# Kernel tuning notes

Measured on AMD Instinct MI355X. Metric: run time of the kernel, lower is better.

The kernel has to match this reference:

```python
import jax, jax.numpy as jnp
import numpy as np

N = 10000        # nodes
E = 160000       # edges (before self loops)
F_IN = 4         # n_features
D = 128          # d_model (per-head out channels for GAT, GCN width)
H = 8            # n_heads
NEG_SLOPE = 0.2  # PyG GATConv default leaky relu slope


def setup_inputs() -> dict:
    key = jax.random.key(0)
    ks = jax.random.split(key, 10)
    x = jax.random.normal(ks[0], (N, F_IN), dtype=jnp.float32)
    edge_index = jax.random.randint(ks[1], (2, E), 0, N, dtype=jnp.int64)
    s = 0.05
    gat_w = jax.random.normal(ks[2], (F_IN, H * D), dtype=jnp.float32) * s
    att_src = jax.random.normal(ks[3], (H, D), dtype=jnp.float32) * s
    att_dst = jax.random.normal(ks[4], (H, D), dtype=jnp.float32) * s
    gat_b = jnp.zeros((H * D,), dtype=jnp.float32)
    gcn1_w = jax.random.normal(ks[5], (H * D, D), dtype=jnp.float32) * s
    gcn1_b = jnp.zeros((D,), dtype=jnp.float32)
    gcn2_w = jax.random.normal(ks[6], (D, D), dtype=jnp.float32) * s
    gcn2_b = jnp.zeros((D,), dtype=jnp.float32)
    return {"x": x, "edge_index": edge_index, "gat_w": gat_w,
            "att_src": att_src, "att_dst": att_dst, "gat_b": gat_b,
            "gcn1_w": gcn1_w, "gcn1_b": gcn1_b,
            "gcn2_w": gcn2_w, "gcn2_b": gcn2_b}


def _add_self_loops(edge_index, n):
    loops = jnp.arange(n, dtype=edge_index.dtype)
    src = jnp.concatenate([edge_index[0], loops])
    dst = jnp.concatenate([edge_index[1], loops])
    return src, dst


def _gat_conv(x, src, dst, w, att_src, att_dst, b):
    # PyG GATConv, concat=True: h [N,H,D]
    h = (x @ w).reshape(-1, H, D)
    a_s = jnp.einsum('nhd,hd->nh', h, att_src)   # per-node src score
    a_d = jnp.einsum('nhd,hd->nh', h, att_dst)   # per-node dst score
    e = jax.nn.leaky_relu(a_s[src] + a_d[dst], NEG_SLOPE)  # [Etot,H]
    # segment softmax over destination node, per head
    m = jax.ops.segment_max(e, dst, num_segments=N)
    ex = jnp.exp(e - m[dst])
    denom = jax.ops.segment_sum(ex, dst, num_segments=N)
    alpha = ex / denom[dst]                       # [Etot,H]
    msg = h[src] * alpha[:, :, None]              # [Etot,H,D]
    out = jax.ops.segment_sum(msg, dst, num_segments=N)  # [N,H,D]
    return out.reshape(-1, H * D) + b


def _gcn_conv(x, src, dst, w, b):
    # PyG GCNConv with symmetric normalization (self loops already added)
    h = x @ w
    deg = jax.ops.segment_sum(jnp.ones_like(dst, dtype=h.dtype), dst,
                              num_segments=N)
    dinv = jnp.where(deg > 0, jax.lax.rsqrt(deg), 0.0)
    norm = dinv[src] * dinv[dst]                  # [Etot]
    out = jax.ops.segment_sum(h[src] * norm[:, None], dst, num_segments=N)
    return out + b


def reference(x, edge_index, gat_w, att_src, att_dst, gat_b,
              gcn1_w, gcn1_b, gcn2_w, gcn2_b):
    src, dst = _add_self_loops(edge_index, N)
    h = _gat_conv(x, src, dst, gat_w, att_src, att_dst, gat_b)
    h = jax.nn.gelu(h, approximate=False)         # torch F.gelu is exact erf
    h = _gcn_conv(h, src, dst, gcn1_w, gcn1_b)
    h = jax.nn.gelu(h, approximate=False)
    h = _gcn_conv(h, src, dst, gcn2_w, gcn2_b)
    return h                                      # [N, D]
```

## Files before the change

### kernel.cpp

```cpp
#include <hip/hip_runtime.h>
#include <math.h>

#define HEADS 8
#define DHEAD 128
#define CMODEL 1024
#define BCAP 64

typedef __attribute__((ext_vector_type(8))) short bf16x8;
typedef __attribute__((ext_vector_type(4))) float f32x4;

__device__ __forceinline__ float gelu_exact(float x) {
    return 0.5f * x * (1.0f + erff(x * 0.70710678118654752440f));
}

__device__ __forceinline__ unsigned short f2bf(float f) {
    unsigned u = __float_as_uint(f);
    return (unsigned short)((u + 0x7FFFu + ((u >> 16) & 1u)) >> 16);
}
__device__ __forceinline__ float bf2f(unsigned short h) {
    return __uint_as_float((unsigned)h << 16);
}

__global__ void __launch_bounds__(256) k_scores(const float* __restrict__ x,
                                                const float* __restrict__ gat_w,
                                                const float* __restrict__ att_src,
                                                const float* __restrict__ att_dst,
                                                const float* __restrict__ W1,
                                                const float* __restrict__ W2,
                                                float* __restrict__ xpack,
                                                float* __restrict__ a_d,
                                                int* __restrict__ cursor,
                                                unsigned short* __restrict__ W1hi,
                                                unsigned short* __restrict__ W1lo,
                                                unsigned short* __restrict__ W2hi,
                                                unsigned short* __restrict__ W2lo,
                                                int n_nodes, int nb_scores) {
    if ((int)blockIdx.x >= nb_scores) {
        int t = (blockIdx.x - nb_scores) * 256 + threadIdx.x;
        const int total1 = (1024 >> 5) * 8 * 64;
        const int total2 = (128 >> 5) * 8 * 64;
        const float* W; unsigned short *Whi, *Wlo;
        if (t < total1) { W = W1; Whi = W1hi; Wlo = W1lo; }
        else if (t < total1 + total2) { t -= total1; W = W2; Whi = W2hi; Wlo = W2lo; }
        else return;
        int lane = t & 63;
        int ct = (t >> 6) & 7;
        int kc = t >> 9;
        int quad = lane >> 4;
        int col = ct * 16 + (lane & 15);
        size_t o = (size_t)t * 8;
        #pragma unroll
        for (int j = 0; j < 8; j++) {
            float w = W[(size_t)(kc * 32 + quad * 8 + j) * 128 + col];
            unsigned short h = f2bf(w);
            Whi[o + j] = h;
            Wlo[o + j] = f2bf(w - bf2f(h));
        }
        return;
    }
    __shared__ float ws_s[32], ws_d[32];
    int t = threadIdx.x;
    if (t < 64) {
        int e = t >> 1;
        int which = t & 1;
        int hh = e >> 2, k = e & 3;
        const float* wrow = gat_w + k * CMODEL + hh * DHEAD;
        const float* av = which ? (att_dst + hh * DHEAD) : (att_src + hh * DHEAD);
        float s = 0.0f;
        for (int c = 0; c < DHEAD; c++) s += wrow[c] * av[c];
        if (which) ws_d[e] = s; else ws_s[e] = s;
    }
    int gid = blockIdx.x * 256 + t;
    if (gid < n_nodes) cursor[gid] = 0;
    __syncthreads();
    int p = gid;
    if (p >= n_nodes * HEADS) return;
    int n = p >> 3, hh = p & 7;
    float4 xv = *(const float4*)(x + (size_t)n * 4);
    float4 ws = *(const float4*)&ws_s[hh * 4];
    float4 wd = *(const float4*)&ws_d[hh * 4];
    a_d[p] = xv.x * wd.x + xv.y * wd.y + xv.z * wd.z + xv.w * wd.w;
    xpack[(size_t)n * 16 + 4 + hh] =
        xv.x * ws.x + xv.y * ws.y + xv.z * ws.z + xv.w * ws.w;
    if (hh == 0) *(float4*)(xpack + (size_t)n * 16) = xv;
}

__global__ void __launch_bounds__(256) k_scatter(const int* __restrict__ ei,
                                                 int* __restrict__ cursor,
                                                 int* __restrict__ bucket,
                                                 int n_nodes, int n_edges) {
    int e = blockIdx.x * 256 + threadIdx.x;
    int etot = n_edges + n_nodes;
    if (e >= etot) return;
    int s, d;
    if (e < n_edges) { s = ei[e]; d = ei[n_edges + e]; }
    else             { s = d = e - n_edges; }
    int pos = atomicAdd(&cursor[d], 1);
    if (pos < BCAP) bucket[(d << 6) + pos] = s;
}

__global__ void __launch_bounds__(256, 3) k_smax_mm1(const float* __restrict__ xpack,
                                                  const float* __restrict__ a_d,
                                                  const int* __restrict__ deg,
                                                  const int* __restrict__ bucket,
                                                  const float* __restrict__ gat_w,
                                                  const float* __restrict__ gat_b,
                                                  const unsigned short* __restrict__ Bhi,
                                                  const unsigned short* __restrict__ Blo,
                                                  float* __restrict__ t,
                                                  int n_nodes) {
    __shared__ float xs[16 * 32];
    __shared__ float ck[2][16 * 68];
    int mb = blockIdx.x;
    int tid = threadIdx.x;
    int lane = tid & 63;
    int w = tid >> 6;

    bf16x8 bhA[2][2], blA[2][2], bhB[2][2], blB[2][2];
    #pragma unroll
    for (int kc2 = 0; kc2 < 2; kc2++)
        #pragma unroll
        for (int ct = 0; ct < 2; ct++) {
            size_t bi = (((size_t)(kc2 * 8) + w * 2 + ct) * 64 + lane) * 8;
            bhA[kc2][ct] = *(const bf16x8*)(Bhi + bi);
            blA[kc2][ct] = *(const bf16x8*)(Blo + bi);
        }

    {
        int q = tid >> 1;
        int half = tid & 1;
        int ln = tid >> 4, hh = q & 7;
        int n = mb * 16 + ln;
        int nc = (n < n_nodes) ? n : (n_nodes - 1);
        int grp = lane & 48;
        int gl = lane & 15;
        int basec = nc << 6;
        int pre0 = bucket[basec + gl];
        int pre1 = bucket[basec + 16 + gl];
        int pre2 = bucket[basec + 32 + gl];
        int pre3 = bucket[basec + 48 + gl];
        auto SRC = [&](int e) -> int {
            int v = (e < 16) ? pre0 : (e < 32) ? pre1 : (e < 48) ? pre2 : pre3;
            return __shfl(v, grp + (e & 15), 64);
        };
        float sum = 0.0f;
        float4 acc = make_float4(0, 0, 0, 0);
        if (n < n_nodes) {
            int dg = deg[n]; if (dg > BCAP) dg = BCAP;
            float ad = a_d[n * 8 + hh];
            int r = half;
            for (; r + 6 < dg; r += 8) {
                int s0 = SRC(r + 0), s1 = SRC(r + 2);
                int s2 = SRC(r + 4), s3 = SRC(r + 6);
                const float* p0 = xpack + (size_t)s0 * 16;
                const float* p1 = xpack + (size_t)s1 * 16;
                const float* p2 = xpack + (size_t)s2 * 16;
                const float* p3 = xpack + (size_t)s3 * 16;
                float e0 = p0[4 + hh] + ad, e1 = p1[4 + hh] + ad;
                float e2 = p2[4 + hh] + ad, e3 = p3[4 + hh] + ad;
                float4 x0 = *(const float4*)p0;
                float4 x1 = *(const float4*)p1;
                float4 x2 = *(const float4*)p2;
                float4 x3 = *(const float4*)p3;
                e0 = (e0 > 0.0f) ? e0 : 0.2f * e0;  float w0 = __expf(e0);
                e1 = (e1 > 0.0f) ? e1 : 0.2f * e1;  float w1 = __expf(e1);
                e2 = (e2 > 0.0f) ? e2 : 0.2f * e2;  float w2 = __expf(e2);
                e3 = (e3 > 0.0f) ? e3 : 0.2f * e3;  float w3 = __expf(e3);
                sum += w0 + w1 + w2 + w3;
                acc.x += w0 * x0.x + w1 * x1.x + w2 * x2.x + w3 * x3.x;
                acc.y += w0 * x0.y + w1 * x1.y + w2 * x2.y + w3 * x3.y;
                acc.z += w0 * x0.z + w1 * x1.z + w2 * x2.z + w3 * x3.z;
                acc.w += w0 * x0.w + w1 * x1.w + w2 * x2.w + w3 * x3.w;
            }
            for (; r < dg; r += 2) {
                int s = SRC(r);
                const float* ps = xpack + (size_t)s * 16;
                float e = ps[4 + hh] + ad;
                e = (e > 0.0f) ? e : 0.2f * e;
                float ex = __expf(e);
                float4 xv = *(const float4*)ps;
                sum += ex;
                acc.x += ex * xv.x; acc.y += ex * xv.y;
                acc.z += ex * xv.z; acc.w += ex * xv.w;
            }
        }
        sum   += __shfl_down(sum, 1);
        acc.x += __shfl_down(acc.x, 1);
        acc.y += __shfl_down(acc.y, 1);
        acc.z += __shfl_down(acc.z, 1);
        acc.w += __shfl_down(acc.w, 1);
        if (half == 0) {
            float inv = (sum > 0.0f) ? (1.0f / sum) : 0.0f;
            *(float4*)&xs[q * 4] = make_float4(acc.x * inv, acc.y * inv,
                                               acc.z * inv, acc.w * inv);
        }
    }
    __syncthreads();

    int lm = lane & 15, quad = lane >> 4;
    int cc = tid & 63;
    int rp = tid >> 6;
    f32x4 macc[2];
    macc[0] = (f32x4){0.0f, 0.0f, 0.0f, 0.0f};
    macc[1] = (f32x4){0.0f, 0.0f, 0.0f, 0.0f};

#define ROUND(RR, BH, BL, BH_N, BL_N, RNEXT)                                    \
    {                                                                           \
        int buf = (RR) & 1;                                                     \
        int col = (RR) * 64 + cc;                                               \
        float w0 = gat_w[col], w1 = gat_w[1024 + col],                          \
              w2 = gat_w[2048 + col], w3 = gat_w[3072 + col];                   \
        float bb = gat_b[col];                                                  \
        int hh2 = (RR) >> 1;                                                    \
        _Pragma("unroll")                                                       \
        for (int rr = 0; rr < 4; rr++) {                                        \
            int row = rp * 4 + rr;                                              \
            float4 xa = *(const float4*)&xs[(row * 8 + hh2) * 4];               \
            float v = xa.x * w0 + xa.y * w1 + xa.z * w2 + xa.w * w3 + bb;       \
            ck[buf][row * 68 + cc] = gelu_exact(v);                             \
        }                                                                       \
        _Pragma("unroll")                                                       \
        for (int kc2 = 0; kc2 < 2; kc2++)                                       \
            _Pragma("unroll")                                                   \
            for (int ct = 0; ct < 2; ct++) {                                    \
                size_t bi = (((size_t)((RNEXT) * 2 + kc2) * 8 + w * 2 + ct) * 64 + lane) * 8; \
                BH_N[kc2][ct] = *(const bf16x8*)(Bhi + bi);                     \
                BL_N[kc2][ct] = *(const bf16x8*)(Blo + bi);                     \
            }                                                                   \
        asm volatile("s_waitcnt lgkmcnt(0)" ::: "memory");                      \
        __builtin_amdgcn_s_barrier();                                           \
        __builtin_amdgcn_sched_barrier(0);                                      \
        _Pragma("unroll")                                                       \
        for (int kc2 = 0; kc2 < 2; kc2++) {                                     \
            float a[8];                                                         \
            *(float4*)&a[0] = *(const float4*)&ck[buf][lm * 68 + kc2 * 32 + quad * 8];     \
            *(float4*)&a[4] = *(const float4*)&ck[buf][lm * 68 + kc2 * 32 + quad * 8 + 4]; \
            bf16x8 ah, al;                                                      \
            _Pragma("unroll")                                                   \
            for (int j = 0; j < 8; j++) {                                       \
                unsigned short h = f2bf(a[j]);                                  \
                ah[j] = (short)h;                                               \
                al[j] = (short)f2bf(a[j] - bf2f(h));                            \
            }                                                                   \
            _Pragma("unroll")                                                   \
            for (int ct = 0; ct < 2; ct++) {                                    \
                macc[ct] = __builtin_amdgcn_mfma_f32_16x16x32_bf16(ah, BH[kc2][ct], macc[ct], 0, 0, 0); \
                macc[ct] = __builtin_amdgcn_mfma_f32_16x16x32_bf16(al, BH[kc2][ct], macc[ct], 0, 0, 0); \
                macc[ct] = __builtin_amdgcn_mfma_f32_16x16x32_bf16(ah, BL[kc2][ct], macc[ct], 0, 0, 0); \
            }                                                                   \
        }                                                                       \
    }

    for (int r = 0; r < 16; r += 2) {
        ROUND(r,     bhA, blA, bhB, blB, r + 1);
        ROUND(r + 1, bhB, blB, bhA, blA, (r + 2 < 16 ? r + 2 : 15));
    }
#undef ROUND

    #pragma unroll
    for (int ct = 0; ct < 2; ct++) {
        int col = (w * 2 + ct) * 16 + lm;
        #pragma unroll
        for (int reg = 0; reg < 4; reg++) {
            int row = mb * 16 + quad * 4 + reg;
            if (row < n_nodes) {
                float dv = 1.0f / sqrtf((float)deg[row]);
                t[(size_t)row * 128 + col] = macc[ct][reg] * dv;
            }
        }
    }
}

__global__ void __launch_bounds__(256) k_mm_mfma(const unsigned short* __restrict__ Afrag_hi,
                                                 const unsigned short* __restrict__ Afrag_lo,
                                                 const unsigned short* __restrict__ Bhi,
                                                 const unsigned short* __restrict__ Blo,
                                                 const int* __restrict__ deg_scale,
                                                 float* __restrict__ outp,
                                                 int n_nodes, int n_mtiles, int kcn) {
    int lane = threadIdx.x & 63;
    int w = threadIdx.x >> 6;
    int colhalf = w >> 1;
    int mtile = blockIdx.x * 2 + (w & 1);
    if (mtile >= n_mtiles) return;

    int lm = lane & 15, quad = lane >> 4;
    f32x4 acc[4];
    #pragma unroll
    for (int ct = 0; ct < 4; ct++) acc[ct] = (f32x4){0.0f, 0.0f, 0.0f, 0.0f};

    const unsigned short* ah_p = Afrag_hi + ((size_t)mtile * kcn * 64 + lane) * 8;
    const unsigned short* al_p = Afrag_lo + ((size_t)mtile * kcn * 64 + lane) * 8;
    const unsigned short* bh_p = Bhi + ((size_t)(colhalf * 4) * 64 + lane) * 8;
    const unsigned short* bl_p = Blo + ((size_t)(colhalf * 4) * 64 + lane) * 8;

    #pragma unroll 4
    for (int kci = 0; kci < kcn; kci++) {
        bf16x8 ah = *(const bf16x8*)(ah_p + (size_t)kci * 512);
        bf16x8 al = *(const bf16x8*)(al_p + (size_t)kci * 512);
        #pragma unroll
        for (int ct = 0; ct < 4; ct++) {
            bf16x8 bh = *(const bf16x8*)(bh_p + (size_t)kci * 4096 + ct * 512);
            bf16x8 bl = *(const bf16x8*)(bl_p + (size_t)kci * 4096 + ct * 512);
            acc[ct] = __builtin_amdgcn_mfma_f32_16x16x32_bf16(ah, bh, acc[ct], 0, 0, 0);
            acc[ct] = __builtin_amdgcn_mfma_f32_16x16x32_bf16(al, bh, acc[ct], 0, 0, 0);
            acc[ct] = __builtin_amdgcn_mfma_f32_16x16x32_bf16(ah, bl, acc[ct], 0, 0, 0);
        }
    }
    #pragma unroll
    for (int ct = 0; ct < 4; ct++) {
        int col = (colhalf * 4 + ct) * 16 + lm;
        #pragma unroll
        for (int reg = 0; reg < 4; reg++) {
            int row = mtile * 16 + quad * 4 + reg;
            if (row < n_nodes) {
                float v = acc[ct][reg] * (1.0f / sqrtf((float)deg_scale[row]));
                outp[(size_t)row * 128 + col] = v;
            }
        }
    }
}

__global__ void __launch_bounds__(256) k_gcn_agg(const float* __restrict__ t,
                                                 const int* __restrict__ deg,
                                                 const int* __restrict__ bucket,
                                                 const float* __restrict__ bias,
                                                 float* __restrict__ outF,
                                                 unsigned short* __restrict__ outHi,
                                                 unsigned short* __restrict__ outLo,
                                                 int n_nodes, int mode) {
    int c = threadIdx.x & 31;
    int ln = threadIdx.x >> 5;
    int n = blockIdx.x * 8 + ln;
    int col0 = blockIdx.y * 64;
    if (n >= n_nodes) return;
    float2 acc = make_float2(0.0f, 0.0f);
    int dgt = deg[n];
    int dg = dgt > BCAP ? BCAP : dgt;
    int base = n << 6;
    int sa = bucket[base + c];
    int sb = bucket[base + 32 + c];
    const float* tp = t + col0 + c * 2;
    int d1 = dg > 32 ? 32 : dg;
    int r = 0;
    for (; r + 4 <= d1; r += 4) {
        int s0 = __shfl(sa, r + 0, 32);
        int s1 = __shfl(sa, r + 1, 32);
        int s2 = __shfl(sa, r + 2, 32);
        int s3 = __shfl(sa, r + 3, 32);
        float2 v0 = *(const float2*)(tp + (size_t)s0 * 128);
        float2 v1 = *(const float2*)(tp + (size_t)s1 * 128);
        float2 v2 = *(const float2*)(tp + (size_t)s2 * 128);
        float2 v3 = *(const float2*)(tp + (size_t)s3 * 128);
        acc.x += v0.x + v1.x + v2.x + v3.x;
        acc.y += v0.y + v1.y + v2.y + v3.y;
    }
    for (; r < d1; r++) {
        int s = __shfl(sa, r, 32);
        float2 v = *(const float2*)(tp + (size_t)s * 128);
        acc.x += v.x; acc.y += v.y;
    }
    for (; r < dg; r++) {
        int s = __shfl(sb, r - 32, 32);
        float2 v = *(const float2*)(tp + (size_t)s * 128);
        acc.x += v.x; acc.y += v.y;
    }
    float dn = 1.0f / sqrtf((float)dgt);
    int k = col0 + c * 2;
    float2 bb = *(const float2*)(bias + k);
    float vx = acc.x * dn + bb.x;
    float vy = acc.y * dn + bb.y;
    if (mode) {
        vx = gelu_exact(vx); vy = gelu_exact(vy);
        size_t o = (((size_t)(n >> 4) * 4 + (k >> 5)) * 64
                    + ((k >> 3) & 3) * 16 + (n & 15)) * 8 + (k & 7);
        unsigned short hx = f2bf(vx), hy = f2bf(vy);
        outHi[o] = hx; outHi[o + 1] = hy;
        outLo[o] = f2bf(vx - bf2f(hx));
        outLo[o + 1] = f2bf(vy - bf2f(hy));
    } else {
        *(float2*)(outF + (size_t)n * 128 + k) = make_float2(vx, vy);
    }
}

extern "C" void kernel_launch(void* const* d_in, const int* in_sizes, int n_in,
                              void* d_out, int out_size, void* d_ws, size_t ws_size,
                              hipStream_t stream) {
    const float* x        = (const float*)d_in[0];
    const int*   ei       = (const int*)d_in[1];
    const float* gat_w    = (const float*)d_in[2];
    const float* att_src  = (const float*)d_in[3];
    const float* att_dst  = (const float*)d_in[4];
    const float* gat_b    = (const float*)d_in[5];
    const float* gcn1_w   = (const float*)d_in[6];
    const float* gcn1_b   = (const float*)d_in[7];
    const float* gcn2_w   = (const float*)d_in[8];
    const float* gcn2_b   = (const float*)d_in[9];
    float* out = (float*)d_out;

    int N = in_sizes[0] / 4;
    int E = in_sizes[1] / 2;
    int Etot = E + N;
    int n_mtiles = (N + 15) / 16;

    char* base = (char*)d_ws;
    float*          t      = (float*)(base);
    float*          t2     = (float*)(base + 5120000);
    unsigned short* out2hi = (unsigned short*)(base + 10240000);
    unsigned short* out2lo = (unsigned short*)(base + 12800000);
    unsigned short* w1hi   = (unsigned short*)(base + 26000000);
    unsigned short* w1lo   = (unsigned short*)(base + 26262144);
    unsigned short* w2hi   = (unsigned short*)(base + 26524288);
    unsigned short* w2lo   = (unsigned short*)(base + 26557056);
    size_t off = 81920000;
    float* xpack  = (float*)(base + off); off += (size_t)N * 16 * 4;
    float* a_d    = (float*)(base + off); off += (size_t)N * 8 * 4;
    int*   cursor = (int*)(base + off);   off += (size_t)N * 4;
    int*   bucket = (int*)(base + off);   off += (size_t)N * BCAP * 4;

    int nb_scores = (N * HEADS + 255) / 256;
    int nb_wswz   = (16384 + 2048 + 255) / 256;

    k_scores<<<nb_scores + nb_wswz, 256, 0, stream>>>(x, gat_w, att_src, att_dst,
                                                      gcn1_w, gcn2_w, xpack, a_d, cursor,
                                                      w1hi, w1lo, w2hi, w2lo, N, nb_scores);

    k_scatter<<<(Etot + 255) / 256, 256, 0, stream>>>(ei, cursor, bucket, N, E);

    k_smax_mm1<<<n_mtiles, 256, 0, stream>>>(xpack, a_d, cursor, bucket,
                                             gat_w, gat_b, w1hi, w1lo, t, N);

    int nmb2 = (n_mtiles + 1) / 2;
    int nagg = (N + 7) / 8;

    k_gcn_agg<<<dim3(nagg, 2), 256, 0, stream>>>(t, cursor, bucket, gcn1_b,
                                                 nullptr, out2hi, out2lo, N, 1);

    k_mm_mfma<<<dim3(nmb2, 1), 256, 0, stream>>>(out2hi, out2lo, w2hi, w2lo,
                                                 cursor, t2, N, n_mtiles, 4);

    k_gcn_agg<<<dim3(nagg, 2), 256, 0, stream>>>(t2, cursor, bucket, gcn2_b,
                                                 out, nullptr, nullptr, N, 0);
}
```

Measured before the change: 157.0 us.

## Split GAT softmax aggregation out of the first GEMM kernel

Moves the GAT edge-softmax aggregation from the fused k_smax_mm1 into a separate k_gat_agg kernel. The new kernel uses 4 threads per (node, head) instead of 2, and writes the aggregated 4-feature inputs to a workspace buffer. k_mm1 then just loads that tile into shared memory. The goal is more parallelism for the gather part and less register pressure in the MFMA kernel. The cost is an extra launch and a small global round trip.

```diff
diff --git a/kernel.cpp b/kernel.cpp
--- a/kernel.cpp
+++ b/kernel.cpp
@@ -99,16 +99,94 @@
     if (pos < BCAP) bucket[(d << 6) + pos] = s;
 }
 
-__global__ void __launch_bounds__(256, 3) k_smax_mm1(const float* __restrict__ xpack,
-                                                  const float* __restrict__ a_d,
-                                                  const int* __restrict__ deg,
-                                                  const int* __restrict__ bucket,
-                                                  const float* __restrict__ gat_w,
-                                                  const float* __restrict__ gat_b,
-                                                  const unsigned short* __restrict__ Bhi,
-                                                  const unsigned short* __restrict__ Blo,
-                                                  float* __restrict__ t,
-                                                  int n_nodes) {
+__global__ void __launch_bounds__(256) k_gat_agg(const float* __restrict__ xpack,
+                                                 const float* __restrict__ a_d,
+                                                 const int* __restrict__ deg,
+                                                 const int* __restrict__ bucket,
+                                                 float* __restrict__ xagg,
+                                                 int n_nodes) {
+    int tid = threadIdx.x;
+    int lane = tid & 63;
+    int ln = tid >> 5;
+    int g = lane & 31;
+    int hh = g >> 2;
+    int quarter = g & 3;
+    int n = blockIdx.x * 8 + ln;
+    int nc = (n < n_nodes) ? n : (n_nodes - 1);
+    int basec = nc << 6;
+    int sa = bucket[basec + g];
+    int sb = bucket[basec + 32 + g];
+    int grp = lane & 32;
+    auto SRC = [&](int e) -> int {
+        int v = (e < 32) ? sa : sb;
+        return __shfl(v, grp + (e & 31), 64);
+    };
+    float sum = 0.0f;
+    float4 acc = make_float4(0, 0, 0, 0);
+    if (n < n_nodes) {
+        int dg = deg[n]; if (dg > BCAP) dg = BCAP;
+        float ad = a_d[n * 8 + hh];
+        int r = quarter;
+        for (; r + 12 < dg; r += 16) {
+            int s0 = SRC(r + 0), s1 = SRC(r + 4);
+            int s2 = SRC(r + 8), s3 = SRC(r + 12);
+            const float* p0 = xpack + (size_t)s0 * 16;
+            const float* p1 = xpack + (size_t)s1 * 16;
+            const float* p2 = xpack + (size_t)s2 * 16;
+            const float* p3 = xpack + (size_t)s3 * 16;
+            float e0 = p0[4 + hh] + ad, e1 = p1[4 + hh] + ad;
+            float e2 = p2[4 + hh] + ad, e3 = p3[4 + hh] + ad;
+            float4 x0 = *(const float4*)p0;
+            float4 x1 = *(const float4*)p1;
+            float4 x2 = *(const float4*)p2;
+            float4 x3 = *(const float4*)p3;
+            e0 = (e0 > 0.0f) ? e0 : 0.2f * e0;  float w0 = __expf(e0);
+            e1 = (e1 > 0.0f) ? e1 : 0.2f * e1;  float w1 = __expf(e1);
+            e2 = (e2 > 0.0f) ? e2 : 0.2f * e2;  float w2 = __expf(e2);
+            e3 = (e3 > 0.0f) ? e3 : 0.2f * e3;  float w3 = __expf(e3);
+            sum += w0 + w1 + w2 + w3;
+            acc.x += w0 * x0.x + w1 * x1.x + w2 * x2.x + w3 * x3.x;
+            acc.y += w0 * x0.y + w1 * x1.y + w2 * x2.y + w3 * x3.y;
+            acc.z += w0 * x0.z + w1 * x1.z + w2 * x2.z + w3 * x3.z;
+            acc.w += w0 * x0.w + w1 * x1.w + w2 * x2.w + w3 * x3.w;
+        }
+        for (; r < dg; r += 4) {
+            int s = SRC(r);
+            const float* ps = xpack + (size_t)s * 16;
+            float e = ps[4 + hh] + ad;
+            e = (e > 0.0f) ? e : 0.2f * e;
+            float ex = __expf(e);
+            float4 xv = *(const float4*)ps;
+            sum += ex;
+            acc.x += ex * xv.x; acc.y += ex * xv.y;
+            acc.z += ex * xv.z; acc.w += ex * xv.w;
+        }
+    }
+    sum   += __shfl_down(sum, 1);
+    acc.x += __shfl_down(acc.x, 1);
+    acc.y += __shfl_down(acc.y, 1);
+    acc.z += __shfl_down(acc.z, 1);
+    acc.w += __shfl_down(acc.w, 1);
+    sum   += __shfl_down(sum, 2);
+    acc.x += __shfl_down(acc.x, 2);
+    acc.y += __shfl_down(acc.y, 2);
+    acc.z += __shfl_down(acc.z, 2);
+    acc.w += __shfl_down(acc.w, 2);
+    if (quarter == 0 && n < n_nodes) {
+        float inv = (sum > 0.0f) ? (1.0f / sum) : 0.0f;
+        *(float4*)&xagg[(size_t)n * 32 + hh * 4] =
+            make_float4(acc.x * inv, acc.y * inv, acc.z * inv, acc.w * inv);
+    }
+}
+
+__global__ void __launch_bounds__(256, 3) k_mm1(const float* __restrict__ xagg,
+                                                const int* __restrict__ deg,
+                                                const float* __restrict__ gat_w,
+                                                const float* __restrict__ gat_b,
+                                                const unsigned short* __restrict__ Bhi,
+                                                const unsigned short* __restrict__ Blo,
+                                                float* __restrict__ t,
+                                                int n_nodes) {
     __shared__ float xs[16 * 32];
     __shared__ float ck[2][16 * 68];
     int mb = blockIdx.x;
@@ -126,74 +204,11 @@
             blA[kc2][ct] = *(const bf16x8*)(Blo + bi);
         }
 
-    {
-        int q = tid >> 1;
-        int half = tid & 1;
-        int ln = tid >> 4, hh = q & 7;
-        int n = mb * 16 + ln;
-        int nc = (n < n_nodes) ? n : (n_nodes - 1);
-        int grp = lane & 48;
-        int gl = lane & 15;
-        int basec = nc << 6;
-        int pre0 = bucket[basec + gl];
-        int pre1 = bucket[basec + 16 + gl];
-        int pre2 = bucket[basec + 32 + gl];
-        int pre3 = bucket[basec + 48 + gl];
-        auto SRC = [&](int e) -> int {
-            int v = (e < 16) ? pre0 : (e < 32) ? pre1 : (e < 48) ? pre2 : pre3;
-            return __shfl(v, grp + (e & 15), 64);
-        };
-        float sum = 0.0f;
-        float4 acc = make_float4(0, 0, 0, 0);
-        if (n < n_nodes) {
-            int dg = deg[n]; if (dg > BCAP) dg = BCAP;
-            float ad = a_d[n * 8 + hh];
-            int r = half;
-            for (; r + 6 < dg; r += 8) {
-                int s0 = SRC(r + 0), s1 = SRC(r + 2);
-                int s2 = SRC(r + 4), s3 = SRC(r + 6);
-                const float* p0 = xpack + (size_t)s0 * 16;
-                const float* p1 = xpack + (size_t)s1 * 16;
-                const float* p2 = xpack + (size_t)s2 * 16;
-                const float* p3 = xpack + (size_t)s3 * 16;
-                float e0 = p0[4 + hh] + ad, e1 = p1[4 + hh] + ad;
-                float e2 = p2[4 + hh] + ad, e3 = p3[4 + hh] + ad;
-                float4 x0 = *(const float4*)p0;
-                float4 x1 = *(const float4*)p1;
-                float4 x2 = *(const float4*)p2;
-                float4 x3 = *(const float4*)p3;
-                e0 = (e0 > 0.0f) ? e0 : 0.2f * e0;  float w0 = __expf(e0);
-                e1 = (e1 > 0.0f) ? e1 : 0.2f * e1;  float w1 = __expf(e1);
-                e2 = (e2 > 0.0f) ? e2 : 0.2f * e2;  float w2 = __expf(e2);
-                e3 = (e3 > 0.0f) ? e3 : 0.2f * e3;  float w3 = __expf(e3);
-                sum += w0 + w1 + w2 + w3;
-                acc.x += w0 * x0.x + w1 * x1.x + w2 * x2.x + w3 * x3.x;
-                acc.y += w0 * x0.y + w1 * x1.y + w2 * x2.y + w3 * x3.y;
-                acc.z += w0 * x0.z + w1 * x1.z + w2 * x2.z + w3 * x3.z;
-                acc.w += w0 * x0.w + w1 * x1.w + w2 * x2.w + w3 * x3.w;
-            }
-            for (; r < dg; r += 2) {
-                int s = SRC(r);
-                const float* ps = xpack + (size_t)s * 16;
-                float e = ps[4 + hh] + ad;
-                e = (e > 0.0f) ? e : 0.2f * e;
-                float ex = __expf(e);
-                float4 xv = *(const float4*)ps;
-                sum += ex;
-                acc.x += ex * xv.x; acc.y += ex * xv.y;
-                acc.z += ex * xv.z; acc.w += ex * xv.w;
-            }
-        }
-        sum   += __shfl_down(sum, 1);
-        acc.x += __shfl_down(acc.x, 1);
-        acc.y += __shfl_down(acc.y, 1);
-        acc.z += __shfl_down(acc.z, 1);
-        acc.w += __shfl_down(acc.w, 1);
-        if (half == 0) {
-            float inv = (sum > 0.0f) ? (1.0f / sum) : 0.0f;
-            *(float4*)&xs[q * 4] = make_float4(acc.x * inv, acc.y * inv,
-                                               acc.z * inv, acc.w * inv);
-        }
+    if (tid < 128) {
+        int idx = mb * 512 + tid * 4;
+        float4 v = make_float4(0, 0, 0, 0);
+        if (idx + 3 < n_nodes * 32) v = *(const float4*)&xagg[idx];
+        *(float4*)&xs[tid * 4] = v;
     }
     __syncthreads();
 
@@ -412,6 +427,7 @@
     unsigned short* w1lo   = (unsigned short*)(base + 26262144);
     unsigned short* w2hi   = (unsigned short*)(base + 26524288);
     unsigned short* w2lo   = (unsigned short*)(base + 26557056);
+    float*          xagg   = (float*)(base + 27000000);
     size_t off = 81920000;
     float* xpack  = (float*)(base + off); off += (size_t)N * 16 * 4;
     float* a_d    = (float*)(base + off); off += (size_t)N * 8 * 4;
@@ -427,8 +443,9 @@
 
     k_scatter<<<(Etot + 255) / 256, 256, 0, stream>>>(ei, cursor, bucket, N, E);
 
-    k_smax_mm1<<<n_mtiles, 256, 0, stream>>>(xpack, a_d, cursor, bucket,
-                                             gat_w, gat_b, w1hi, w1lo, t, N);
+    k_gat_agg<<<(N + 7) / 8, 256, 0, stream>>>(xpack, a_d, cursor, bucket, xagg, N);
+
+    k_mm1<<<n_mtiles, 256, 0, stream>>>(xagg, cursor, gat_w, gat_b, w1hi, w1lo, t, N);
 
     int nmb2 = (n_mtiles + 1) / 2;
     int nagg = (N + 7) / 8;
```

Measured after the change: 160.3 us. 2.1% more time.

## Fuse GCN1 aggregation with GCN2 matmul through shared memory

Applied to the files above, without the earlier changes.

Merges the first GCN aggregation (with bias and GELU) and the following 128x128 MFMA matmul into one kernel. Each block aggregates 16 nodes into LDS, then splits them into bf16 hi/lo fragments on the fly and runs the MFMA. This removes the global round trip of the hi/lo intermediate and one kernel launch. In exchange, each block now does the irregular gather and the MFMA in sequence, and occupancy depends on the 512-thread blocks.

```diff
diff --git a/kernel.cpp b/kernel.cpp
--- a/kernel.cpp
+++ b/kernel.cpp
@@ -271,52 +271,90 @@
     }
 }
 
-__global__ void __launch_bounds__(256) k_mm_mfma(const unsigned short* __restrict__ Afrag_hi,
-                                                 const unsigned short* __restrict__ Afrag_lo,
-                                                 const unsigned short* __restrict__ Bhi,
-                                                 const unsigned short* __restrict__ Blo,
-                                                 const int* __restrict__ deg_scale,
-                                                 float* __restrict__ outp,
-                                                 int n_nodes, int n_mtiles, int kcn) {
-    int lane = threadIdx.x & 63;
-    int w = threadIdx.x >> 6;
-    int colhalf = w >> 1;
-    int mtile = blockIdx.x * 2 + (w & 1);
-    if (mtile >= n_mtiles) return;
-
+__global__ void __launch_bounds__(512) k_gcn1_fused(const float* __restrict__ t,
+                                                    const int* __restrict__ deg,
+                                                    const int* __restrict__ bucket,
+                                                    const float* __restrict__ bias,
+                                                    const unsigned short* __restrict__ Bhi,
+                                                    const unsigned short* __restrict__ Blo,
+                                                    float* __restrict__ t2,
+                                                    int n_nodes) {
+    __shared__ float hs[16][132];
+    int tid = threadIdx.x;
+    int mb = blockIdx.x;
+    int c = tid & 31;
+    int ln = tid >> 5;
+    int node = mb * 16 + ln;
+    int nc = (node < n_nodes) ? node : (n_nodes - 1);
+    int base = nc << 6;
+    int sa = bucket[base + c];
+    int sb = bucket[base + 32 + c];
+    int dgt = (node < n_nodes) ? deg[node] : 1;
+    int dg = dgt > BCAP ? BCAP : dgt;
+    float dn = 1.0f / sqrtf((float)dgt);
+    int d1 = dg > 32 ? 32 : dg;
+    #pragma unroll
+    for (int h2 = 0; h2 < 2; h2++) {
+        const float* tp = t + h2 * 64 + c * 2;
+        float2 acc = make_float2(0.0f, 0.0f);
+        int r = 0;
+        for (; r + 4 <= d1; r += 4) {
+            int s0 = __shfl(sa, r + 0, 32);
+            int s1 = __shfl(sa, r + 1, 32);
+            int s2 = __shfl(sa, r + 2, 32);
+            int s3 = __shfl(sa, r + 3, 32);
+            float2 v0 = *(const float2*)(tp + (size_t)s0 * 128);
+            float2 v1 = *(const float2*)(tp + (size_t)s1 * 128);
+            float2 v2 = *(const float2*)(tp + (size_t)s2 * 128);
+            float2 v3 = *(const float2*)(tp + (size_t)s3 * 128);
+            acc.x += v0.x + v1.x + v2.x + v3.x;
+            acc.y += v0.y + v1.y + v2.y + v3.y;
+        }
+        for (; r < d1; r++) {
+            int s = __shfl(sa, r, 32);
+            float2 v = *(const float2*)(tp + (size_t)s * 128);
+            acc.x += v.x; acc.y += v.y;
+        }
+        for (; r < dg; r++) {
+            int s = __shfl(sb, r - 32, 32);
+            float2 v = *(const float2*)(tp + (size_t)s * 128);
+            acc.x += v.x; acc.y += v.y;
+        }
+        int k = h2 * 64 + c * 2;
+        float2 bb = *(const float2*)(bias + k);
+        hs[ln][k]     = gelu_exact(acc.x * dn + bb.x);
+        hs[ln][k + 1] = gelu_exact(acc.y * dn + bb.y);
+    }
+    __syncthreads();
+    int lane = tid & 63;
+    int w = tid >> 6;
     int lm = lane & 15, quad = lane >> 4;
-    f32x4 acc[4];
+    f32x4 acc2 = (f32x4){0.0f, 0.0f, 0.0f, 0.0f};
     #pragma unroll
-    for (int ct = 0; ct < 4; ct++) acc[ct] = (f32x4){0.0f, 0.0f, 0.0f, 0.0f};
-
-    const unsigned short* ah_p = Afrag_hi + ((size_t)mtile * kcn * 64 + lane) * 8;
-    const unsigned short* al_p = Afrag_lo + ((size_t)mtile * kcn * 64 + lane) * 8;
-    const unsigned short* bh_p = Bhi + ((size_t)(colhalf * 4) * 64 + lane) * 8;
-    const unsigned short* bl_p = Blo + ((size_t)(colhalf * 4) * 64 + lane) * 8;
-
-    #pragma unroll 4
-    for (int kci = 0; kci < kcn; kci++) {
-        bf16x8 ah = *(const bf16x8*)(ah_p + (size_t)kci * 512);
-        bf16x8 al = *(const bf16x8*)(al_p + (size_t)kci * 512);
+    for (int kc = 0; kc < 4; kc++) {
+        float a[8];
+        *(float4*)&a[0] = *(const float4*)&hs[lm][kc * 32 + quad * 8];
+        *(float4*)&a[4] = *(const float4*)&hs[lm][kc * 32 + quad * 8 + 4];
+        bf16x8 ah, al;
         #pragma unroll
-        for (int ct = 0; ct < 4; ct++) {
-            bf16x8 bh = *(const bf16x8*)(bh_p + (size_t)kci * 4096 + ct * 512);
-            bf16x8 bl = *(const bf16x8*)(bl_p + (size_t)kci * 4096 + ct * 512);
-            acc[ct] = __builtin_amdgcn_mfma_f32_16x16x32_bf16(ah, bh, acc[ct], 0, 0, 0);
-            acc[ct] = __builtin_amdgcn_mfma_f32_16x16x32_bf16(al, bh, acc[ct], 0, 0, 0);
-            acc[ct] = __builtin_amdgcn_mfma_f32_16x16x32_bf16(ah, bl, acc[ct], 0, 0, 0);
-        }
-    }
+        for (int j = 0; j < 8; j++) {
+            unsigned short h = f2bf(a[j]);
+            ah[j] = (short)h;
+            al[j] = (short)f2bf(a[j] - bf2f(h));
+        }
+        bf16x8 bh = *(const bf16x8*)(Bhi + (((size_t)(kc * 8 + w)) * 64 + lane) * 8);
+        bf16x8 bl = *(const bf16x8*)(Blo + (((size_t)(kc * 8 + w)) * 64 + lane) * 8);
+        acc2 = __builtin_amdgcn_mfma_f32_16x16x32_bf16(ah, bh, acc2, 0, 0, 0);
+        acc2 = __builtin_amdgcn_mfma_f32_16x16x32_bf16(al, bh, acc2, 0, 0, 0);
+        acc2 = __builtin_amdgcn_mfma_f32_16x16x32_bf16(ah, bl, acc2, 0, 0, 0);
+    }
+    int col = w * 16 + lm;
     #pragma unroll
-    for (int ct = 0; ct < 4; ct++) {
-        int col = (colhalf * 4 + ct) * 16 + lm;
-        #pragma unroll
-        for (int reg = 0; reg < 4; reg++) {
-            int row = mtile * 16 + quad * 4 + reg;
-            if (row < n_nodes) {
-                float v = acc[ct][reg] * (1.0f / sqrtf((float)deg_scale[row]));
-                outp[(size_t)row * 128 + col] = v;
-            }
+    for (int reg = 0; reg < 4; reg++) {
+        int row = mb * 16 + quad * 4 + reg;
+        if (row < n_nodes) {
+            float dv = 1.0f / sqrtf((float)deg[row]);
+            t2[(size_t)row * 128 + col] = acc2[reg] * dv;
         }
     }
 }
@@ -326,9 +364,7 @@
                                                  const int* __restrict__ bucket,
                                                  const float* __restrict__ bias,
                                                  float* __restrict__ outF,
-                                                 unsigned short* __restrict__ outHi,
-                                                 unsigned short* __restrict__ outLo,
-                                                 int n_nodes, int mode) {
+                                                 int n_nodes) {
     int c = threadIdx.x & 31;
     int ln = threadIdx.x >> 5;
     int n = blockIdx.x * 8 + ln;
@@ -368,19 +404,8 @@
     float dn = 1.0f / sqrtf((float)dgt);
     int k = col0 + c * 2;
     float2 bb = *(const float2*)(bias + k);
-    float vx = acc.x * dn + bb.x;
-    float vy = acc.y * dn + bb.y;
-    if (mode) {
-        vx = gelu_exact(vx); vy = gelu_exact(vy);
-        size_t o = (((size_t)(n >> 4) * 4 + (k >> 5)) * 64
-                    + ((k >> 3) & 3) * 16 + (n & 15)) * 8 + (k & 7);
-        unsigned short hx = f2bf(vx), hy = f2bf(vy);
-        outHi[o] = hx; outHi[o + 1] = hy;
-        outLo[o] = f2bf(vx - bf2f(hx));
-        outLo[o + 1] = f2bf(vy - bf2f(hy));
-    } else {
-        *(float2*)(outF + (size_t)n * 128 + k) = make_float2(vx, vy);
-    }
+    *(float2*)(outF + (size_t)n * 128 + k) =
+        make_float2(acc.x * dn + bb.x, acc.y * dn + bb.y);
 }
 
 extern "C" void kernel_launch(void* const* d_in, const int* in_sizes, int n_in,
@@ -406,8 +431,6 @@
     char* base = (char*)d_ws;
     float*          t      = (float*)(base);
     float*          t2     = (float*)(base + 5120000);
-    unsigned short* out2hi = (unsigned short*)(base + 10240000);
-    unsigned short* out2lo = (unsigned short*)(base + 12800000);
     unsigned short* w1hi   = (unsigned short*)(base + 26000000);
     unsigned short* w1lo   = (unsigned short*)(base + 26262144);
     unsigned short* w2hi   = (unsigned short*)(base + 26524288);
@@ -430,15 +453,9 @@
     k_smax_mm1<<<n_mtiles, 256, 0, stream>>>(xpack, a_d, cursor, bucket,
                                              gat_w, gat_b, w1hi, w1lo, t, N);
 
-    int nmb2 = (n_mtiles + 1) / 2;
-    int nagg = (N + 7) / 8;
-
-    k_gcn_agg<<<dim3(nagg, 2), 256, 0, stream>>>(t, cursor, bucket, gcn1_b,
-                                                 nullptr, out2hi, out2lo, N, 1);
-
-    k_mm_mfma<<<dim3(nmb2, 1), 256, 0, stream>>>(out2hi, out2lo, w2hi, w2lo,
-                                                 cursor, t2, N, n_mtiles, 4);
-
-    k_gcn_agg<<<dim3(nagg, 2), 256, 0, stream>>>(t2, cursor, bucket, gcn2_b,
-                                                 out, nullptr, nullptr, N, 0);
-}
+    k_gcn1_fused<<<n_mtiles, 512, 0, stream>>>(t, cursor, bucket, gcn1_b,
+                                               w2hi, w2lo, t2, N);
+
+    k_gcn_agg<<<dim3((N + 7) / 8, 2), 256, 0, stream>>>(t2, cursor, bucket, gcn2_b,
+                                                        out, N);
+}
```

After: 153.1 us. -2.5%, faster.
